# Kernel optimization log

Measured on AMD Instinct MI355X. Metric: run time of the kernel, lower is better.

Reference implementation:

```python
import jax, jax.numpy as jnp
import numpy as np

B, NQ, NK = 4, 2048, 2048
DQ = DK = DV = 256
H = 8
HD = DV // H
EPS = 1e-5


def _ln(x, g, b):
    m = jnp.mean(x, axis=-1, keepdims=True)
    v = jnp.mean(jnp.square(x - m), axis=-1, keepdims=True)
    return (x - m) * jax.lax.rsqrt(v + EPS) * g + b


def setup_inputs() -> dict:
    key = jax.random.key(0)
    ks = jax.random.split(key, 12)
    s = 0.02
    return {
        "Q": jax.random.normal(ks[0], (B, NQ, DQ), jnp.float32),
        "K": jax.random.normal(ks[1], (B, NK, DK), jnp.float32),
        "Wq": jax.random.normal(ks[2], (DV, DQ), jnp.float32) * s,
        "bq": jnp.zeros((DV,), jnp.float32),
        "Wk": jax.random.normal(ks[3], (DV, DK), jnp.float32) * s,
        "bk": jnp.zeros((DV,), jnp.float32),
        "Wv": jax.random.normal(ks[4], (DV, DK), jnp.float32) * s,
        "bv": jnp.zeros((DV,), jnp.float32),
        "Wo": jax.random.normal(ks[5], (DV, DV), jnp.float32) * s,
        "bo": jnp.zeros((DV,), jnp.float32),
        "g0": jnp.ones((DV,), jnp.float32),
        "b0": jnp.zeros((DV,), jnp.float32),
        "g1": jnp.ones((DV,), jnp.float32),
        "b1": jnp.zeros((DV,), jnp.float32),
    }


def reference(Q, K, Wq, bq, Wk, bk, Wv, bv, Wo, bo, g0, b0, g1, b1):
    Qp = Q @ Wq.T + bq            # [B,NQ,DV]
    Kp = K @ Wk.T + bk            # [B,NK,DV]
    Vp = K @ Wv.T + bv            # [B,NK,DV]
    # split(head_dim, dim=2) + cat(dim=0) == reshape heads from contiguous channel chunks
    qh = Qp.reshape(B, NQ, H, HD)
    kh = Kp.reshape(B, NK, H, HD)
    vh = Vp.reshape(B, NK, H, HD)
    scores = jnp.einsum("bqhd,bkhd->bhqk", qh, kh) / jnp.sqrt(jnp.float32(HD))
    attn = jax.nn.softmax(scores, axis=-1)          # [B,H,NQ,NK]
    o = jnp.einsum("bhqk,bkhd->bqhd", attn, vh).reshape(B, NQ, DV)
    o = _ln(o, g0, b0)
    out = o + jax.nn.relu(o @ Wo.T + bo)
    out = _ln(out, g1, b1)
    return out
```

## Files before the change

### kernel.cpp

```cpp
#include <hip/hip_runtime.h>
#include <hip/hip_bf16.h>
#include <math.h>

#define DV 256
#define NH 8
#define NB 4
#define NQ 2048
#define NKK 2048

typedef __attribute__((ext_vector_type(8))) short s8v;
typedef __attribute__((ext_vector_type(16))) float fx16;

typedef const __attribute__((address_space(1))) char g1c;
typedef __attribute__((address_space(3))) char l3c;

__device__ __forceinline__ void gl_lds16(const void* g, void* l) {
    __builtin_amdgcn_global_load_lds((g1c*)g, (l3c*)l, 16, 0, 0);
}
__device__ __forceinline__ unsigned cvtpk_bf16(float lo, float hi) {
    unsigned r;
    asm("v_cvt_pk_bf16_f32 %0, %1, %2" : "=v"(r) : "v"(lo), "v"(hi));
    return r;
}
__device__ __forceinline__ ushort f2bf(float x) {
    unsigned u = __builtin_bit_cast(unsigned, x);
    return (ushort)((u + 0x7fffu + ((u >> 16) & 1u)) >> 16);
}
__device__ __forceinline__ float bf2f(ushort h) {
    return __builtin_bit_cast(float, (unsigned)h << 16);
}

__global__ __launch_bounds__(256) void prep_k(
    const float* __restrict__ Q, const float* __restrict__ K,
    const float* __restrict__ Wq, const float* __restrict__ Wk,
    const float* __restrict__ Wv, const float* __restrict__ Wo,
    ushort* __restrict__ Qc, ushort* __restrict__ Kc, ushort* __restrict__ Wf)
{
    const int i = blockIdx.x * 256 + threadIdx.x;
    const float* src;
    ushort* dst;
    if (i < 262144) {
        src = Q + (size_t)i * 8;  dst = Qc + (size_t)i * 8;
    } else if (i < 524288) {
        src = K + (size_t)(i - 262144) * 8;  dst = Kc + (size_t)(i - 262144) * 8;
    } else {
        const int j = i - 524288;
        const int w = j >> 13, c = j & 8191;
        const int bn = c >> 11, s = (c >> 8) & 7, cc = c & 255;
        const int colblk = cc >> 7, ks = (cc >> 6) & 1, g5 = (cc >> 5) & 1, l31 = cc & 31;
        const int col = bn * 64 + colblk * 32 + l31;
        const int k = s * 32 + ks * 16 + g5 * 8;
        const float* Wsrc = (w == 0) ? Wq : (w == 1) ? Wk : (w == 2) ? Wv : Wo;
        src = Wsrc + (size_t)col * 256 + k;
        dst = Wf + (size_t)j * 8;
    }
    float4 a = *(const float4*)src;
    float4 b = *(const float4*)(src + 4);
    uint4 pk;
    pk.x = cvtpk_bf16(a.x, a.y); pk.y = cvtpk_bf16(a.z, a.w);
    pk.z = cvtpk_bf16(b.x, b.y); pk.w = cvtpk_bf16(b.z, b.w);
    *(uint4*)dst = pk;
}

#define GEMM_MFMA_BODY(A_, WF_)                                                         \
    __shared__ __align__(16) char lds[2][12288];                                        \
    const int t = threadIdx.x, lane = t & 63, wv = t >> 6;                              \
    const int l31 = lane & 31, g5 = lane >> 5;                                          \
    const int bm = blockIdx.x, bn = blockIdx.y;                                         \
    const ushort* asrc0 = A_ + (size_t)(bm * 128 + (t >> 7) * 32 + (t & 31)) * 256      \
                             + ((t >> 6) & 1) * 16 + ((t >> 5) & 1) * 8;                \
    const ushort* asrc1 = asrc0 + 64 * 256;                                             \
    const ushort* wsrc  = WF_ + (size_t)(bn * 8) * 2048 + t * 8;                        \
    gl_lds16(asrc0, &lds[0][wv * 1024]);                                                \
    gl_lds16(asrc1, &lds[0][4096 + wv * 1024]);                                         \
    gl_lds16(wsrc,  &lds[0][8192 + wv * 1024]);                                         \
    __syncthreads();                                                                    \
    fx16 acc0 = {}, acc1 = {};                                                          \
    for (int s = 0; s < 8; ++s) {                                                       \
        const int buf = s & 1;                                                          \
        if (s + 1 < 8) {                                                                \
            gl_lds16(asrc0 + (s + 1) * 32, &lds[buf ^ 1][wv * 1024]);                   \
            gl_lds16(asrc1 + (s + 1) * 32, &lds[buf ^ 1][4096 + wv * 1024]);            \
            gl_lds16(wsrc + (s + 1) * 2048, &lds[buf ^ 1][8192 + wv * 1024]);           \
        }                                                                               \
        const char* Al = lds[buf];                                                      \
        const char* Wl = lds[buf] + 8192;                                               \
        s8v a0  = *(const s8v*)(Al + (wv * 2 + 0) * 1024 + lane * 16);                  \
        s8v a1  = *(const s8v*)(Al + (wv * 2 + 1) * 1024 + lane * 16);                  \
        s8v b00 = *(const s8v*)(Wl + 0 * 1024 + lane * 16);                             \
        s8v b01 = *(const s8v*)(Wl + 1 * 1024 + lane * 16);                             \
        s8v b10 = *(const s8v*)(Wl + 2 * 1024 + lane * 16);                             \
        s8v b11 = *(const s8v*)(Wl + 3 * 1024 + lane * 16);                             \
        __builtin_amdgcn_s_setprio(1);                                                  \
        acc0 = __builtin_amdgcn_mfma_f32_32x32x16_bf16(a0, b00, acc0, 0, 0, 0);         \
        acc0 = __builtin_amdgcn_mfma_f32_32x32x16_bf16(a1, b01, acc0, 0, 0, 0);         \
        acc1 = __builtin_amdgcn_mfma_f32_32x32x16_bf16(a0, b10, acc1, 0, 0, 0);         \
        acc1 = __builtin_amdgcn_mfma_f32_32x32x16_bf16(a1, b11, acc1, 0, 0, 0);         \
        __builtin_amdgcn_s_setprio(0);                                                  \
        __syncthreads();                                                                \
    }                                                                                   \
    const int row_b = bm * 128 + wv * 32;

__global__ __launch_bounds__(256) void gemm_qkv_k(
    const ushort* __restrict__ Qc, const ushort* __restrict__ Kc,
    const ushort* __restrict__ Wf,
    const float* __restrict__ bq, const float* __restrict__ bk, const float* __restrict__ bv,
    ushort* __restrict__ Qb, ushort* __restrict__ Kb, ushort* __restrict__ Vt)
{
    const int z = blockIdx.z;
    const ushort* A  = (z == 0) ? Qc : Kc;
    const ushort* WF = Wf + (size_t)z * 65536;
    const float* bias = (z == 0) ? bq : (z == 1) ? bk : bv;
    GEMM_MFMA_BODY(A, WF)
    const float bs0 = bias[bn * 64 + l31];
    const float bs1 = bias[bn * 64 + 32 + l31];
    if (z < 2) {
        ushort* O = (z == 0) ? Qb : Kb;
#pragma unroll
        for (int r = 0; r < 16; ++r) {
            const int row_g = row_b + (r & 3) + 8 * (r >> 2) + 4 * g5;
            O[(size_t)row_g * 256 + bn * 64 + l31]      = f2bf(acc0[r] + bs0);
            O[(size_t)row_g * 256 + bn * 64 + 32 + l31] = f2bf(acc1[r] + bs1);
        }
    } else {
#pragma unroll
        for (int r = 0; r < 16; ++r) {
            const int row_g = row_b + (r & 3) + 8 * (r >> 2) + 4 * g5;
            const int bb = row_g >> 11, n = row_g & 2047;
            Vt[((size_t)(bb * 8 + bn * 2 + 0) * 32 + l31) * 2048 + n] = f2bf(acc0[r] + bs0);
            Vt[((size_t)(bb * 8 + bn * 2 + 1) * 32 + l31) * 2048 + n] = f2bf(acc1[r] + bs1);
        }
    }
}

__global__ __launch_bounds__(256) void gemm_tail_k(
    const ushort* __restrict__ Ain, const ushort* __restrict__ Wfo,
    const float* __restrict__ bias, float* __restrict__ Out)
{
    GEMM_MFMA_BODY(Ain, Wfo)
    const float bs0 = bias[bn * 64 + l31];
    const float bs1 = bias[bn * 64 + 32 + l31];
#pragma unroll
    for (int r = 0; r < 16; ++r) {
        const int row_g = row_b + (r & 3) + 8 * (r >> 2) + 4 * g5;
        Out[(size_t)row_g * 256 + bn * 64 + l31]      = acc0[r] + bs0;
        Out[(size_t)row_g * 256 + bn * 64 + 32 + l31] = acc1[r] + bs1;
    }
}

__global__ __launch_bounds__(256) void flash_mfma_k(
    const ushort* __restrict__ Qb, const ushort* __restrict__ Kb,
    const ushort* __restrict__ Vt, ushort* __restrict__ Osb, float* __restrict__ L)
{
    __shared__ __align__(16) char lds[2][8192];
    const int t = threadIdx.x;
    const int lane = t & 63, wv = t >> 6;
    const int l31 = lane & 31, g5 = lane >> 5;
    const int qt = blockIdx.x, h = blockIdx.y;
    const int b = blockIdx.z >> 1, sp = blockIdx.z & 1;
    const float CE = 0.17677669529663687f * 1.4426950408889634f;

    s8v qf0, qf1;
    {
        const ushort* qp = Qb + (((size_t)b * NQ + qt * 128 + wv * 32 + l31) << 8) + h * 32 + g5 * 8;
        qf0 = *(const s8v*)(qp);
        qf1 = *(const s8v*)(qp + 16);
    }
    s8v ones;
#pragma unroll
    for (int j = 0; j < 8; ++j) ones[j] = (short)0x3F80;

    const ushort* ksrc = Kb + (((size_t)b * NKK + sp * 1024 + ((t >> 7) * 32 + (t & 31))) << 8)
                            + h * 32 + ((t >> 6) & 1) * 16 + ((t >> 5) & 1) * 8;
    const ushort* vsrc = Vt + (((size_t)(b * NH + h) * 32 + (t & 31)) << 11) + sp * 1024
                            + (t >> 6) * 16 + ((t >> 5) & 1) * 8;

    fx16 O0 = {}, lsum = {};

    gl_lds16(ksrc, &lds[0][wv * 1024]);
    gl_lds16(vsrc, &lds[0][4096 + wv * 1024]);
    __syncthreads();

    for (int kt = 0; kt < 16; ++kt) {
        const int buf = kt & 1;
        if (kt + 1 < 16) {
            gl_lds16(ksrc + (size_t)(kt + 1) * 64 * DV, &lds[buf ^ 1][wv * 1024]);
            gl_lds16(vsrc + (kt + 1) * 64, &lds[buf ^ 1][4096 + wv * 1024]);
        }
        const char* Kl = lds[buf];
        const char* Vl = lds[buf] + 4096;
        s8v kf00 = *(const s8v*)(Kl + 0 * 1024 + lane * 16);
        s8v kf01 = *(const s8v*)(Kl + 1 * 1024 + lane * 16);
        s8v kf10 = *(const s8v*)(Kl + 2 * 1024 + lane * 16);
        s8v kf11 = *(const s8v*)(Kl + 3 * 1024 + lane * 16);
        s8v vfa[4];
        vfa[0] = *(const s8v*)(Vl + 0 * 1024 + lane * 16);
        vfa[1] = *(const s8v*)(Vl + 1 * 1024 + lane * 16);
        vfa[2] = *(const s8v*)(Vl + 2 * 1024 + lane * 16);
        vfa[3] = *(const s8v*)(Vl + 3 * 1024 + lane * 16);

        fx16 z = {};
        __builtin_amdgcn_s_setprio(1);
        fx16 Sa = __builtin_amdgcn_mfma_f32_32x32x16_bf16(kf00, qf0, z, 0, 0, 0);
        Sa = __builtin_amdgcn_mfma_f32_32x32x16_bf16(kf01, qf1, Sa, 0, 0, 0);
        fx16 Sb = __builtin_amdgcn_mfma_f32_32x32x16_bf16(kf10, qf0, z, 0, 0, 0);
        Sb = __builtin_amdgcn_mfma_f32_32x32x16_bf16(kf11, qf1, Sb, 0, 0, 0);
        __builtin_amdgcn_s_setprio(0);

        float p[32];
#pragma unroll
        for (int i = 0; i < 16; ++i) {
            p[i]      = __builtin_amdgcn_exp2f(Sa[i] * CE);
            p[16 + i] = __builtin_amdgcn_exp2f(Sb[i] * CE);
        }

        __builtin_amdgcn_s_setprio(1);
#pragma unroll
        for (int kt2 = 0; kt2 < 4; ++kt2) {
            const int pb = 8 * kt2;
            auto ra = __builtin_amdgcn_permlane32_swap(
                cvtpk_bf16(p[pb + 0], p[pb + 1]), cvtpk_bf16(p[pb + 4], p[pb + 5]), false, false);
            auto rb = __builtin_amdgcn_permlane32_swap(
                cvtpk_bf16(p[pb + 2], p[pb + 3]), cvtpk_bf16(p[pb + 6], p[pb + 7]), false, false);
            union { unsigned u[4]; s8v v; } pf;
            pf.u[0] = ra[0]; pf.u[1] = rb[0]; pf.u[2] = ra[1]; pf.u[3] = rb[1];
            O0   = __builtin_amdgcn_mfma_f32_32x32x16_bf16(vfa[kt2], pf.v, O0, 0, 0, 0);
            lsum = __builtin_amdgcn_mfma_f32_32x32x16_bf16(ones,    pf.v, lsum, 0, 0, 0);
        }
        __builtin_amdgcn_s_setprio(0);
        __syncthreads();
    }

    {
        const int qrow = qt * 128 + wv * 32 + l31;
        ushort* dst0 = Osb + (size_t)sp * (8192 * 256)
                     + (((size_t)b * NQ + qrow) << 8) + h * 32 + g5 * 4;
#pragma unroll
        for (int rr = 0; rr < 4; ++rr) {
            uint2 w;
            w.x = cvtpk_bf16(O0[4 * rr + 0], O0[4 * rr + 1]);
            w.y = cvtpk_bf16(O0[4 * rr + 2], O0[4 * rr + 3]);
            *(uint2*)(dst0 + 8 * rr) = w;
        }
        if (g5 == 0)
            L[(((size_t)sp * NB + b) * NH + h) * NQ + qrow] = lsum[0];
    }
}

__global__ __launch_bounds__(256) void comb_ln_k(
    const ushort* __restrict__ Osb, const float* __restrict__ L,
    const float* __restrict__ g, const float* __restrict__ bb,
    float* __restrict__ Y, ushort* __restrict__ Yb)
{
    const int t = threadIdx.x, lane = t & 63, w = t >> 6;
    const int row = blockIdx.x * 4 + w;
    const int b = row >> 11, q = row & 2047;
    const int h = lane >> 3;
    const size_t lbase = (((size_t)b * NH + h) * NQ + q);
    const float l0 = L[lbase];
    const float l1 = L[(size_t)NB * NH * NQ + lbase];
    const float inv = 1.f / (l0 + l1);
    const ushort4 x0 = *(const ushort4*)(Osb + (size_t)row * 256 + lane * 4);
    const ushort4 x1 = *(const ushort4*)(Osb + (size_t)(8192 * 256) + (size_t)row * 256 + lane * 4);
    float4 x;
    x.x = (bf2f(x0.x) + bf2f(x1.x)) * inv;
    x.y = (bf2f(x0.y) + bf2f(x1.y)) * inv;
    x.z = (bf2f(x0.z) + bf2f(x1.z)) * inv;
    x.w = (bf2f(x0.w) + bf2f(x1.w)) * inv;
    float s  = (x.x + x.y) + (x.z + x.w);
    float sq = fmaf(x.x, x.x, fmaf(x.y, x.y, fmaf(x.z, x.z, x.w * x.w)));
    for (int off = 32; off; off >>= 1) {
        s  += __shfl_xor(s, off);
        sq += __shfl_xor(sq, off);
    }
    const float mean = s * (1.f / 256.f);
    const float var  = sq * (1.f / 256.f) - mean * mean;
    const float ri   = rsqrtf(var + 1e-5f);
    const float4 gv = *(const float4*)(g + lane * 4);
    const float4 bv = *(const float4*)(bb + lane * 4);
    float4 y;
    y.x = (x.x - mean) * ri * gv.x + bv.x;
    y.y = (x.y - mean) * ri * gv.y + bv.y;
    y.z = (x.z - mean) * ri * gv.z + bv.z;
    y.w = (x.w - mean) * ri * gv.w + bv.w;
    *(float4*)(Y + (size_t)row * 256 + lane * 4) = y;
    uint2 p;
    p.x = cvtpk_bf16(y.x, y.y);
    p.y = cvtpk_bf16(y.z, y.w);
    *(uint2*)(Yb + (size_t)row * 256 + lane * 4) = p;
}

__global__ __launch_bounds__(256) void ln_res_k(
    const float* __restrict__ Hh, const float* __restrict__ T,
    const float* __restrict__ g, const float* __restrict__ bb, float* __restrict__ Y)
{
    const int t = threadIdx.x, lane = t & 63, w = t >> 6;
    const int row = blockIdx.x * 4 + w;
    const float4 hv = *(const float4*)(Hh + (size_t)row * 256 + lane * 4);
    const float4 tv = *(const float4*)(T + (size_t)row * 256 + lane * 4);
    float4 x;
    x.x = hv.x + fmaxf(tv.x, 0.f);
    x.y = hv.y + fmaxf(tv.y, 0.f);
    x.z = hv.z + fmaxf(tv.z, 0.f);
    x.w = hv.w + fmaxf(tv.w, 0.f);
    float s  = (x.x + x.y) + (x.z + x.w);
    float sq = fmaf(x.x, x.x, fmaf(x.y, x.y, fmaf(x.z, x.z, x.w * x.w)));
    for (int off = 32; off; off >>= 1) {
        s  += __shfl_xor(s, off);
        sq += __shfl_xor(sq, off);
    }
    const float mean = s * (1.f / 256.f);
    const float var  = sq * (1.f / 256.f) - mean * mean;
    const float ri   = rsqrtf(var + 1e-5f);
    const float4 gv = *(const float4*)(g + lane * 4);
    const float4 bv = *(const float4*)(bb + lane * 4);
    float4 y;
    y.x = (x.x - mean) * ri * gv.x + bv.x;
    y.y = (x.y - mean) * ri * gv.y + bv.y;
    y.z = (x.z - mean) * ri * gv.z + bv.z;
    y.w = (x.w - mean) * ri * gv.w + bv.w;
    *(float4*)(Y + (size_t)row * 256 + lane * 4) = y;
}

extern "C" void kernel_launch(void* const* d_in, const int* in_sizes, int n_in,
                              void* d_out, int out_size, void* d_ws, size_t ws_size,
                              hipStream_t stream) {
    const float* Q  = (const float*)d_in[0];
    const float* K  = (const float*)d_in[1];
    const float* Wq = (const float*)d_in[2];
    const float* bq = (const float*)d_in[3];
    const float* Wk = (const float*)d_in[4];
    const float* bk = (const float*)d_in[5];
    const float* Wv = (const float*)d_in[6];
    const float* bv = (const float*)d_in[7];
    const float* Wo = (const float*)d_in[8];
    const float* bo = (const float*)d_in[9];
    const float* g0 = (const float*)d_in[10];
    const float* b0 = (const float*)d_in[11];
    const float* g1 = (const float*)d_in[12];
    const float* b1 = (const float*)d_in[13];
    float* out = (float*)d_out;

    char* wsb = (char*)d_ws;
    const size_t MB = 1u << 20;
    ushort* Qc  = (ushort*)(wsb + 14 * MB);
    ushort* Kc  = (ushort*)(wsb + 18 * MB);
    ushort* Wf  = (ushort*)(wsb + 13 * MB);
    ushort* Qb  = (ushort*)(wsb + 1 * MB);
    ushort* Kb  = (ushort*)(wsb + 5 * MB);
    ushort* Vt  = (ushort*)(wsb + 9 * MB);
    ushort* Osb = (ushort*)(wsb + 14 * MB);
    float*  L   = (float*)(wsb + 30 * MB);
    float*  h0  = (float*)(wsb + 1 * MB);
    ushort* h0b = (ushort*)(wsb + 9 * MB);
    float*  t1  = (float*)(wsb + 22 * MB);

    prep_k<<<2176, 256, 0, stream>>>(Q, K, Wq, Wk, Wv, Wo, Qc, Kc, Wf);
    gemm_qkv_k<<<dim3(64, 4, 3), 256, 0, stream>>>(Qc, Kc, Wf, bq, bk, bv, Qb, Kb, Vt);
    flash_mfma_k<<<dim3(16, 8, 8), 256, 0, stream>>>(Qb, Kb, Vt, Osb, L);
    comb_ln_k<<<2048, 256, 0, stream>>>(Osb, L, g0, b0, h0, h0b);
    gemm_tail_k<<<dim3(64, 4), 256, 0, stream>>>(h0b, Wf + 3 * 65536, bo, t1);
    ln_res_k<<<2048, 256, 0, stream>>>(h0, t1, g1, b1, out);
}
```

Baseline: 77.13 us.

## Fuse output GEMM with residual LayerNorm, split KV four ways, prescale Q

Folds the softmax scale into the Q projection epilogue so the flash kernel skips a multiply per score. It raises the KV split from 2 to 4 for more flash blocks, with the combine kernel summing four partials. It also replaces the tail GEMM plus residual-LayerNorm kernels with one kernel that reuses the bf16 h0 tile from LDS, dropping the fp32 h0 and t1 round trips. The trade-offs are a bf16 residual input, more partial-output traffic, and only 128 blocks in the fused GEMM.

```diff
diff --git a/kernel.cpp b/kernel.cpp
--- a/kernel.cpp
+++ b/kernel.cpp
@@ -112,15 +112,22 @@
     const ushort* WF = Wf + (size_t)z * 65536;
     const float* bias = (z == 0) ? bq : (z == 1) ? bk : bv;
     GEMM_MFMA_BODY(A, WF)
+    const float CE = 0.17677669529663687f * 1.4426950408889634f;
     const float bs0 = bias[bn * 64 + l31];
     const float bs1 = bias[bn * 64 + 32 + l31];
-    if (z < 2) {
-        ushort* O = (z == 0) ? Qb : Kb;
+    if (z == 0) {
 #pragma unroll
         for (int r = 0; r < 16; ++r) {
             const int row_g = row_b + (r & 3) + 8 * (r >> 2) + 4 * g5;
-            O[(size_t)row_g * 256 + bn * 64 + l31]      = f2bf(acc0[r] + bs0);
-            O[(size_t)row_g * 256 + bn * 64 + 32 + l31] = f2bf(acc1[r] + bs1);
+            Qb[(size_t)row_g * 256 + bn * 64 + l31]      = f2bf((acc0[r] + bs0) * CE);
+            Qb[(size_t)row_g * 256 + bn * 64 + 32 + l31] = f2bf((acc1[r] + bs1) * CE);
+        }
+    } else if (z == 1) {
+#pragma unroll
+        for (int r = 0; r < 16; ++r) {
+            const int row_g = row_b + (r & 3) + 8 * (r >> 2) + 4 * g5;
+            Kb[(size_t)row_g * 256 + bn * 64 + l31]      = f2bf(acc0[r] + bs0);
+            Kb[(size_t)row_g * 256 + bn * 64 + 32 + l31] = f2bf(acc1[r] + bs1);
         }
     } else {
 #pragma unroll
@@ -130,21 +137,6 @@
             Vt[((size_t)(bb * 8 + bn * 2 + 0) * 32 + l31) * 2048 + n] = f2bf(acc0[r] + bs0);
             Vt[((size_t)(bb * 8 + bn * 2 + 1) * 32 + l31) * 2048 + n] = f2bf(acc1[r] + bs1);
         }
-    }
-}
-
-__global__ __launch_bounds__(256) void gemm_tail_k(
-    const ushort* __restrict__ Ain, const ushort* __restrict__ Wfo,
-    const float* __restrict__ bias, float* __restrict__ Out)
-{
-    GEMM_MFMA_BODY(Ain, Wfo)
-    const float bs0 = bias[bn * 64 + l31];
-    const float bs1 = bias[bn * 64 + 32 + l31];
-#pragma unroll
-    for (int r = 0; r < 16; ++r) {
-        const int row_g = row_b + (r & 3) + 8 * (r >> 2) + 4 * g5;
-        Out[(size_t)row_g * 256 + bn * 64 + l31]      = acc0[r] + bs0;
-        Out[(size_t)row_g * 256 + bn * 64 + 32 + l31] = acc1[r] + bs1;
     }
 }
 
@@ -157,8 +149,7 @@
     const int lane = t & 63, wv = t >> 6;
     const int l31 = lane & 31, g5 = lane >> 5;
     const int qt = blockIdx.x, h = blockIdx.y;
-    const int b = blockIdx.z >> 1, sp = blockIdx.z & 1;
-    const float CE = 0.17677669529663687f * 1.4426950408889634f;
+    const int b = blockIdx.z >> 2, sp = blockIdx.z & 3;
 
     s8v qf0, qf1;
     {
@@ -170,9 +161,9 @@
 #pragma unroll
     for (int j = 0; j < 8; ++j) ones[j] = (short)0x3F80;
 
-    const ushort* ksrc = Kb + (((size_t)b * NKK + sp * 1024 + ((t >> 7) * 32 + (t & 31))) << 8)
+    const ushort* ksrc = Kb + (((size_t)b * NKK + sp * 512 + ((t >> 7) * 32 + (t & 31))) << 8)
                             + h * 32 + ((t >> 6) & 1) * 16 + ((t >> 5) & 1) * 8;
-    const ushort* vsrc = Vt + (((size_t)(b * NH + h) * 32 + (t & 31)) << 11) + sp * 1024
+    const ushort* vsrc = Vt + (((size_t)(b * NH + h) * 32 + (t & 31)) << 11) + sp * 512
                             + (t >> 6) * 16 + ((t >> 5) & 1) * 8;
 
     fx16 O0 = {}, lsum = {};
@@ -181,9 +172,9 @@
     gl_lds16(vsrc, &lds[0][4096 + wv * 1024]);
     __syncthreads();
 
-    for (int kt = 0; kt < 16; ++kt) {
+    for (int kt = 0; kt < 8; ++kt) {
         const int buf = kt & 1;
-        if (kt + 1 < 16) {
+        if (kt + 1 < 8) {
             gl_lds16(ksrc + (size_t)(kt + 1) * 64 * DV, &lds[buf ^ 1][wv * 1024]);
             gl_lds16(vsrc + (kt + 1) * 64, &lds[buf ^ 1][4096 + wv * 1024]);
         }
@@ -210,8 +201,8 @@
         float p[32];
 #pragma unroll
         for (int i = 0; i < 16; ++i) {
-            p[i]      = __builtin_amdgcn_exp2f(Sa[i] * CE);
-            p[16 + i] = __builtin_amdgcn_exp2f(Sb[i] * CE);
+            p[i]      = __builtin_amdgcn_exp2f(Sa[i]);
+            p[16 + i] = __builtin_amdgcn_exp2f(Sb[i]);
         }
 
         __builtin_amdgcn_s_setprio(1);
@@ -250,76 +241,154 @@
 __global__ __launch_bounds__(256) void comb_ln_k(
     const ushort* __restrict__ Osb, const float* __restrict__ L,
     const float* __restrict__ g, const float* __restrict__ bb,
-    float* __restrict__ Y, ushort* __restrict__ Yb)
+    ushort* __restrict__ Yb)
 {
     const int t = threadIdx.x, lane = t & 63, w = t >> 6;
     const int row = blockIdx.x * 4 + w;
     const int b = row >> 11, q = row & 2047;
     const int h = lane >> 3;
     const size_t lbase = (((size_t)b * NH + h) * NQ + q);
-    const float l0 = L[lbase];
-    const float l1 = L[(size_t)NB * NH * NQ + lbase];
-    const float inv = 1.f / (l0 + l1);
-    const ushort4 x0 = *(const ushort4*)(Osb + (size_t)row * 256 + lane * 4);
-    const ushort4 x1 = *(const ushort4*)(Osb + (size_t)(8192 * 256) + (size_t)row * 256 + lane * 4);
+    const size_t LS = (size_t)NB * NH * NQ;
+    const float lt = (L[lbase] + L[LS + lbase]) + (L[2 * LS + lbase] + L[3 * LS + lbase]);
+    const float inv = 1.f / lt;
+    const size_t SZS = (size_t)8192 * 256;
+    const size_t off = (size_t)row * 256 + lane * 4;
+    const ushort4 x0 = *(const ushort4*)(Osb + off);
+    const ushort4 x1 = *(const ushort4*)(Osb + SZS + off);
+    const ushort4 x2 = *(const ushort4*)(Osb + 2 * SZS + off);
+    const ushort4 x3 = *(const ushort4*)(Osb + 3 * SZS + off);
     float4 x;
-    x.x = (bf2f(x0.x) + bf2f(x1.x)) * inv;
-    x.y = (bf2f(x0.y) + bf2f(x1.y)) * inv;
-    x.z = (bf2f(x0.z) + bf2f(x1.z)) * inv;
-    x.w = (bf2f(x0.w) + bf2f(x1.w)) * inv;
+    x.x = ((bf2f(x0.x) + bf2f(x1.x)) + (bf2f(x2.x) + bf2f(x3.x))) * inv;
+    x.y = ((bf2f(x0.y) + bf2f(x1.y)) + (bf2f(x2.y) + bf2f(x3.y))) * inv;
+    x.z = ((bf2f(x0.z) + bf2f(x1.z)) + (bf2f(x2.z) + bf2f(x3.z))) * inv;
+    x.w = ((bf2f(x0.w) + bf2f(x1.w)) + (bf2f(x2.w) + bf2f(x3.w))) * inv;
     float s  = (x.x + x.y) + (x.z + x.w);
     float sq = fmaf(x.x, x.x, fmaf(x.y, x.y, fmaf(x.z, x.z, x.w * x.w)));
-    for (int off = 32; off; off >>= 1) {
-        s  += __shfl_xor(s, off);
-        sq += __shfl_xor(sq, off);
+    for (int off2 = 32; off2; off2 >>= 1) {
+        s  += __shfl_xor(s, off2);
+        sq += __shfl_xor(sq, off2);
     }
     const float mean = s * (1.f / 256.f);
     const float var  = sq * (1.f / 256.f) - mean * mean;
     const float ri   = rsqrtf(var + 1e-5f);
     const float4 gv = *(const float4*)(g + lane * 4);
     const float4 bv = *(const float4*)(bb + lane * 4);
-    float4 y;
-    y.x = (x.x - mean) * ri * gv.x + bv.x;
-    y.y = (x.y - mean) * ri * gv.y + bv.y;
-    y.z = (x.z - mean) * ri * gv.z + bv.z;
-    y.w = (x.w - mean) * ri * gv.w + bv.w;
-    *(float4*)(Y + (size_t)row * 256 + lane * 4) = y;
     uint2 p;
-    p.x = cvtpk_bf16(y.x, y.y);
-    p.y = cvtpk_bf16(y.z, y.w);
+    p.x = cvtpk_bf16((x.x - mean) * ri * gv.x + bv.x, (x.y - mean) * ri * gv.y + bv.y);
+    p.y = cvtpk_bf16((x.z - mean) * ri * gv.z + bv.z, (x.w - mean) * ri * gv.w + bv.w);
     *(uint2*)(Yb + (size_t)row * 256 + lane * 4) = p;
 }
 
-__global__ __launch_bounds__(256) void ln_res_k(
-    const float* __restrict__ Hh, const float* __restrict__ T,
-    const float* __restrict__ g, const float* __restrict__ bb, float* __restrict__ Y)
+__global__ __launch_bounds__(256) void gemm_ln_k(
+    const ushort* __restrict__ Ain, const ushort* __restrict__ Wfo,
+    const float* __restrict__ bo, const float* __restrict__ g1,
+    const float* __restrict__ b1, float* __restrict__ out)
 {
-    const int t = threadIdx.x, lane = t & 63, w = t >> 6;
-    const int row = blockIdx.x * 4 + w;
-    const float4 hv = *(const float4*)(Hh + (size_t)row * 256 + lane * 4);
-    const float4 tv = *(const float4*)(T + (size_t)row * 256 + lane * 4);
-    float4 x;
-    x.x = hv.x + fmaxf(tv.x, 0.f);
-    x.y = hv.y + fmaxf(tv.y, 0.f);
-    x.z = hv.z + fmaxf(tv.z, 0.f);
-    x.w = hv.w + fmaxf(tv.w, 0.f);
-    float s  = (x.x + x.y) + (x.z + x.w);
-    float sq = fmaf(x.x, x.x, fmaf(x.y, x.y, fmaf(x.z, x.z, x.w * x.w)));
-    for (int off = 32; off; off >>= 1) {
-        s  += __shfl_xor(s, off);
-        sq += __shfl_xor(sq, off);
-    }
-    const float mean = s * (1.f / 256.f);
-    const float var  = sq * (1.f / 256.f) - mean * mean;
-    const float ri   = rsqrtf(var + 1e-5f);
-    const float4 gv = *(const float4*)(g + lane * 4);
-    const float4 bv = *(const float4*)(bb + lane * 4);
-    float4 y;
-    y.x = (x.x - mean) * ri * gv.x + bv.x;
-    y.y = (x.y - mean) * ri * gv.y + bv.y;
-    y.z = (x.z - mean) * ri * gv.z + bv.z;
-    y.w = (x.w - mean) * ri * gv.w + bv.w;
-    *(float4*)(Y + (size_t)row * 256 + lane * 4) = y;
+    __shared__ __align__(16) char alds[32768];
+    __shared__ __align__(16) char wlds[2][16384];
+    __shared__ float red[4][64][2];
+    __shared__ float par[64][2];
+    const int t = threadIdx.x, lane = t & 63, wv = t >> 6;
+    const int l31 = lane & 31, g5 = lane >> 5;
+    const int row0 = blockIdx.x * 64;
+
+#pragma unroll
+    for (int it = 0; it < 8; ++it) {
+        const int id = it * 256 + t;
+        const int s = id >> 8, rem = id & 255, kc = rem >> 6, row = rem & 63;
+        gl_lds16(Ain + (size_t)(row0 + row) * 256 + s * 32 + (kc >> 1) * 16 + (kc & 1) * 8,
+                 &alds[id * 16]);
+    }
+#pragma unroll
+    for (int it = 0; it < 4; ++it) {
+        const int id = it * 256 + t;
+        gl_lds16(Wfo + ((size_t)(id >> 8) * 2048 + (id & 255)) * 8, &wlds[0][id * 16]);
+    }
+    __syncthreads();
+
+    fx16 acc[2][2] = {};
+    for (int s = 0; s < 8; ++s) {
+        const int buf = s & 1;
+        if (s + 1 < 8) {
+#pragma unroll
+            for (int it = 0; it < 4; ++it) {
+                const int id = it * 256 + t;
+                gl_lds16(Wfo + ((size_t)(id >> 8) * 2048 + (s + 1) * 256 + (id & 255)) * 8,
+                         &wlds[buf ^ 1][id * 16]);
+            }
+        }
+        s8v a[2][2], bf[2][2];
+#pragma unroll
+        for (int rb = 0; rb < 2; ++rb)
+#pragma unroll
+            for (int ks = 0; ks < 2; ++ks)
+                a[rb][ks] = *(const s8v*)(alds + ((s * 4 + ks * 2 + g5) * 64 + rb * 32 + l31) * 16);
+#pragma unroll
+        for (int ks = 0; ks < 2; ++ks)
+#pragma unroll
+            for (int ch = 0; ch < 2; ++ch)
+                bf[ks][ch] = *(const s8v*)(wlds[buf] + (wv * 256 + ch * 128 + ks * 64 + g5 * 32 + l31) * 16);
+        __builtin_amdgcn_s_setprio(1);
+#pragma unroll
+        for (int rb = 0; rb < 2; ++rb)
+#pragma unroll
+            for (int ch = 0; ch < 2; ++ch) {
+                acc[rb][ch] = __builtin_amdgcn_mfma_f32_32x32x16_bf16(a[rb][0], bf[0][ch], acc[rb][ch], 0, 0, 0);
+                acc[rb][ch] = __builtin_amdgcn_mfma_f32_32x32x16_bf16(a[rb][1], bf[1][ch], acc[rb][ch], 0, 0, 0);
+            }
+        __builtin_amdgcn_s_setprio(0);
+        __syncthreads();
+    }
+
+    const int cg0 = wv * 64 + l31, cg1 = cg0 + 32;
+    const float bo0 = bo[cg0], bo1 = bo[cg1];
+    const int s0 = cg0 >> 5, kk0 = cg0 & 31;
+    const int s1 = cg1 >> 5, kk1 = cg1 & 31;
+    const int coff0 = (s0 * 4 + ((kk0 >> 4) << 1) + ((kk0 >> 3) & 1)) * 64;
+    const int coff1 = (s1 * 4 + ((kk1 >> 4) << 1) + ((kk1 >> 3) & 1)) * 64;
+    float x[2][2][16];
+#pragma unroll
+    for (int rb = 0; rb < 2; ++rb) {
+#pragma unroll
+        for (int r = 0; r < 16; ++r) {
+            const int row = rb * 32 + (r & 3) + 8 * (r >> 2) + 4 * g5;
+            const ushort h0v = *(const ushort*)(alds + ((coff0 + row) << 4) + (kk0 & 7) * 2);
+            const ushort h1v = *(const ushort*)(alds + ((coff1 + row) << 4) + (kk1 & 7) * 2);
+            const float x0 = bf2f(h0v) + fmaxf(acc[rb][0][r] + bo0, 0.f);
+            const float x1 = bf2f(h1v) + fmaxf(acc[rb][1][r] + bo1, 0.f);
+            x[rb][0][r] = x0; x[rb][1][r] = x1;
+            float sv = x0 + x1;
+            float sq = fmaf(x0, x0, x1 * x1);
+#pragma unroll
+            for (int off = 1; off < 32; off <<= 1) {
+                sv += __shfl_xor(sv, off);
+                sq += __shfl_xor(sq, off);
+            }
+            if (l31 == 0) { red[wv][row][0] = sv; red[wv][row][1] = sq; }
+        }
+    }
+    __syncthreads();
+    if (t < 64) {
+        const float sv = (red[0][t][0] + red[1][t][0]) + (red[2][t][0] + red[3][t][0]);
+        const float sq = (red[0][t][1] + red[1][t][1]) + (red[2][t][1] + red[3][t][1]);
+        const float mean = sv * (1.f / 256.f);
+        const float var  = sq * (1.f / 256.f) - mean * mean;
+        par[t][0] = mean;
+        par[t][1] = rsqrtf(var + 1e-5f);
+    }
+    __syncthreads();
+    const float g1a = g1[cg0], g1b = g1[cg1];
+    const float b1a = b1[cg0], b1b = b1[cg1];
+#pragma unroll
+    for (int rb = 0; rb < 2; ++rb) {
+#pragma unroll
+        for (int r = 0; r < 16; ++r) {
+            const int row = rb * 32 + (r & 3) + 8 * (r >> 2) + 4 * g5;
+            const float mean = par[row][0], ri = par[row][1];
+            out[(size_t)(row0 + row) * 256 + cg0] = (x[rb][0][r] - mean) * ri * g1a + b1a;
+            out[(size_t)(row0 + row) * 256 + cg1] = (x[rb][1][r] - mean) * ri * g1b + b1b;
+        }
+    }
 }
 
 extern "C" void kernel_launch(void* const* d_in, const int* in_sizes, int n_in,
@@ -351,14 +420,11 @@
     ushort* Vt  = (ushort*)(wsb + 9 * MB);
     ushort* Osb = (ushort*)(wsb + 14 * MB);
     float*  L   = (float*)(wsb + 30 * MB);
-    float*  h0  = (float*)(wsb + 1 * MB);
     ushort* h0b = (ushort*)(wsb + 9 * MB);
-    float*  t1  = (float*)(wsb + 22 * MB);
 
     prep_k<<<2176, 256, 0, stream>>>(Q, K, Wq, Wk, Wv, Wo, Qc, Kc, Wf);
     gemm_qkv_k<<<dim3(64, 4, 3), 256, 0, stream>>>(Qc, Kc, Wf, bq, bk, bv, Qb, Kb, Vt);
-    flash_mfma_k<<<dim3(16, 8, 8), 256, 0, stream>>>(Qb, Kb, Vt, Osb, L);
-    comb_ln_k<<<2048, 256, 0, stream>>>(Osb, L, g0, b0, h0, h0b);
-    gemm_tail_k<<<dim3(64, 4), 256, 0, stream>>>(h0b, Wf + 3 * 65536, bo, t1);
-    ln_res_k<<<2048, 256, 0, stream>>>(h0, t1, g1, b1, out);
-}
+    flash_mfma_k<<<dim3(16, 8, 16), 256, 0, stream>>>(Qb, Kb, Vt, Osb, L);
+    comb_ln_k<<<2048, 256, 0, stream>>>(Osb, L, g0, b0, h0b);
+    gemm_ln_k<<<128, 256, 0, stream>>>(h0b, Wf + 3 * 65536, bo, g1, b1, out);
+}
```

Measured after the change: 77.21 us. Within noise of the previous version (+0.1%).
